# Performance work log

Hardware: AMD Instinct MI355X
Metric: run time of the kernel (lower is better)

## Reference

```python
import jax, jax.numpy as jnp
import numpy as np
from jax import lax

B, L = 2, 2048          # batch, seq_len
V = 256                 # vocab
DM = 256                # d_model
DI = 512                # d_inner = 2*d_model (expand=2)
N = 16                  # d_state
R = 16                  # dt_rank = ceil(d_model/16)
K = 4                   # d_conv
NL = 4                  # n_layer
DO = 10                 # d_output
EPS = 1e-5


def setup_inputs() -> dict:
    key = jax.random.key(0)
    ks = jax.random.split(key, 12)
    f = lambda k, shp, s=0.02: (jax.random.normal(k, shp, jnp.float32) * s)
    A_init = jnp.log(jnp.tile(jnp.arange(1, N + 1, dtype=jnp.float32)[None, None, :], (NL, DI, 1)))
    return {
        "input_ids": jax.random.randint(ks[0], (B, L), 0, V, dtype=jnp.int32),
        "emb": f(ks[1], (V, DM)),
        "norm_w": jnp.ones((NL, DM), jnp.float32),
        "norm_b": jnp.zeros((NL, DM), jnp.float32),
        "in_proj_w": f(ks[2], (NL, 2 * DI, DM)),
        "conv_w": f(ks[3], (NL, DI, K), 0.1),
        "conv_b": jnp.zeros((NL, DI), jnp.float32),
        "x_proj_w": f(ks[4], (NL, R + 2 * N, DI)),
        "dt_proj_w": f(ks[5], (NL, DI, R), 0.1),
        "dt_proj_b": f(ks[6], (NL, DI), 0.1),
        "A_log": A_init,
        "Dp": jnp.ones((NL, DI), jnp.float32),
        "out_proj_w": f(ks[7], (NL, DM, DI)),
        "normf_w": jnp.ones((DM,), jnp.float32),
        "normf_b": jnp.zeros((DM,), jnp.float32),
        "dec_w": f(ks[8], (DO, DM)),
        "dec_b": jnp.zeros((DO,), jnp.float32),
    }


def _layer_norm(x, w, b):
    m = x.mean(-1, keepdims=True)
    v = jnp.mean((x - m) ** 2, axis=-1, keepdims=True)
    return (x - m) * lax.rsqrt(v + EPS) * w + b


def _causal_dwconv(x, w, b):
    # x: [B,L,DI], w: [DI,K] depthwise causal conv
    xt = x.transpose(0, 2, 1)  # [B,DI,L]
    out = lax.conv_general_dilated(xt, w[:, None, :], (1,), [(K - 1, 0)],
                                   feature_group_count=DI)
    return (out + b[None, :, None]).transpose(0, 2, 1)


def _selective_scan(deltaA, deltaBu, C):
    # deltaA, deltaBu: [B,L,DI,N]; C: [B,L,N]
    def step(h, inp):
        dA, dBu, c = inp
        h = dA * h + dBu                       # [B,DI,N]
        y = jnp.einsum('bdn,bn->bd', h, c)
        return h, y
    h0 = jnp.zeros(deltaA.shape[:1] + deltaA.shape[2:], deltaA.dtype)
    _, ys = lax.scan(step, h0, (deltaA.transpose(1, 0, 2, 3),
                                deltaBu.transpose(1, 0, 2, 3),
                                C.transpose(1, 0, 2)))
    return ys.transpose(1, 0, 2)  # [B,L,DI]


def _mixer(x, in_w, cw, cb, xp_w, dt_w, dt_b, A_log, Dp, out_w):
    xz = jnp.einsum('bld,ed->ble', x, in_w)        # [B,L,2*DI]
    xm, z = jnp.split(xz, 2, axis=-1)
    xc = jax.nn.silu(_causal_dwconv(xm, cw, cb))   # [B,L,DI]
    x_dbl = jnp.einsum('bld,ed->ble', xc, xp_w)    # [B,L,R+2N]
    dt, Bm, Cm = jnp.split(x_dbl, [R, R + N], axis=-1)
    delta = jax.nn.softplus(jnp.einsum('blr,dr->bld', dt, dt_w) + dt_b)  # [B,L,DI]
    A = -jnp.exp(A_log)                            # [DI,N]
    deltaA = jnp.exp(delta[..., None] * A)         # [B,L,DI,N]
    deltaBu = delta[..., None] * Bm[:, :, None, :] * xc[..., None]
    y = _selective_scan(deltaA, deltaBu, Cm)       # [B,L,DI]
    y = y + Dp * xc
    y = y * jax.nn.silu(z)
    return jnp.einsum('bld,ed->ble', y, out_w)     # [B,L,DM]


def reference(input_ids, emb, norm_w, norm_b, in_proj_w, conv_w, conv_b,
              x_proj_w, dt_proj_w, dt_proj_b, A_log, Dp, out_proj_w,
              normf_w, normf_b, dec_w, dec_b):
    hidden = emb[input_ids]                        # [B,L,DM]
    residual = None
    for i in range(NL):
        residual = hidden + residual if residual is not None else hidden
        h = _layer_norm(residual, norm_w[i], norm_b[i])
        hidden = _mixer(h, in_proj_w[i], conv_w[i], conv_b[i], x_proj_w[i],
                        dt_proj_w[i], dt_proj_b[i], A_log[i], Dp[i], out_proj_w[i])
    residual = hidden + residual
    hidden = _layer_norm(residual, normf_w, normf_b)
    pooled = hidden.mean(axis=1)                   # [B,DM]
    return pooled @ dec_w.T + dec_b                # [B,DO]
```

## Files before the change

kernel.cpp:

```cpp
#include <hip/hip_runtime.h>
#include <hip/hip_bf16.h>

#define BB 2
#define LL 2048
#define DM 256
#define DI 512
#define NST 16
#define RDT 16
#define KC 4
#define NLAY 4
#define DOUT 10
#define XDIM 48
#define TOK (BB*LL)
#define EPSF 1e-5f
#define CHUNK 16
#define NCH (LL/CHUNK)

typedef __bf16 bf16x8 __attribute__((ext_vector_type(8)));
typedef __bf16 bf16x4 __attribute__((ext_vector_type(4)));
typedef float  f32x4  __attribute__((ext_vector_type(4)));

__device__ __forceinline__ float sigmoid_f(float x) { return 1.0f / (1.0f + __expf(-x)); }

__global__ void cast_w_kernel(const float* __restrict__ a, const float* __restrict__ b,
                              const float* __restrict__ c,
                              __bf16* __restrict__ ab, __bf16* __restrict__ bb,
                              __bf16* __restrict__ cbf,
                              int na, int nb, int nc) {
  int stride = gridDim.x * 256;
  for (int i = blockIdx.x*256 + threadIdx.x; i < na; i += stride) ab[i] = (__bf16)a[i];
  for (int i = blockIdx.x*256 + threadIdx.x; i < nb; i += stride) bb[i] = (__bf16)b[i];
  for (int i = blockIdx.x*256 + threadIdx.x; i < nc; i += stride) cbf[i] = (__bf16)c[i];
}

__global__ void add_ln_kernel(float* __restrict__ residual, const float* __restrict__ hidden,
                              const int* __restrict__ ids, const float* __restrict__ emb,
                              const float* __restrict__ w, const float* __restrict__ bia,
                              float* __restrict__ out, __bf16* __restrict__ out_bf,
                              int first, int write32) {
  int wv = threadIdx.x >> 6, lane = threadIdx.x & 63;
  int t = blockIdx.x*4 + wv;
  float4 rv;
  if (first) {
    rv = *(const float4*)&emb[(size_t)ids[t]*DM + lane*4];
  } else {
    float4 h4 = *(const float4*)&hidden[(size_t)t*DM + lane*4];
    float4 o4 = *(const float4*)&residual[(size_t)t*DM + lane*4];
    rv.x = h4.x + o4.x; rv.y = h4.y + o4.y;
    rv.z = h4.z + o4.z; rv.w = h4.w + o4.w;
  }
  *(float4*)&residual[(size_t)t*DM + lane*4] = rv;
  float s = rv.x + rv.y + rv.z + rv.w;
  #pragma unroll
  for (int o = 32; o; o >>= 1) s += __shfl_xor(s, o);
  float mean = s * (1.0f/DM);
  float d0 = rv.x - mean, d1 = rv.y - mean, d2 = rv.z - mean, d3 = rv.w - mean;
  float q = d0*d0 + d1*d1 + d2*d2 + d3*d3;
  #pragma unroll
  for (int o = 32; o; o >>= 1) q += __shfl_xor(q, o);
  float rsig = rsqrtf(q * (1.0f/DM) + EPSF);
  float4 w4 = *(const float4*)&w[lane*4];
  float4 b4 = *(const float4*)&bia[lane*4];
  float v0 = d0*rsig*w4.x + b4.x;
  float v1 = d1*rsig*w4.y + b4.y;
  float v2 = d2*rsig*w4.z + b4.z;
  float v3 = d3*rsig*w4.w + b4.w;
  if (write32) {
    float4 o4; o4.x = v0; o4.y = v1; o4.z = v2; o4.w = v3;
    *(float4*)&out[(size_t)t*DM + lane*4] = o4;
  }
  bf16x4 bv;
  bv[0] = (__bf16)v0; bv[1] = (__bf16)v1; bv[2] = (__bf16)v2; bv[3] = (__bf16)v3;
  *(bf16x4*)&out_bf[(size_t)t*DM + lane*4] = bv;
}

__global__ __launch_bounds__(256, 2) void gemm_in_bf16(const __bf16* __restrict__ A,
                                                       const __bf16* __restrict__ W,
                                                       __bf16* __restrict__ xm,
                                                       __bf16* __restrict__ zg) {
  __shared__ __bf16 As[4*64*8];
  __shared__ __bf16 Ws[8*64*8];
  const int K = DM;
  int tid = threadIdx.x;
  int lane = tid & 63, wv = tid >> 6;
  int bm = blockIdx.y * 64, be = blockIdx.x * 128;
  int ss = tid >> 6, sq = (tid >> 4) & 3, sm = tid & 15;
  f32x4 acc[8];
  #pragma unroll
  for (int et = 0; et < 8; ++et) acc[et] = (f32x4){0.f, 0.f, 0.f, 0.f};
  for (int k0 = 0; k0 < K; k0 += 32) {
    bf16x8 av = *(const bf16x8*)&A[(size_t)(bm + ss*16 + sm)*K + k0 + sq*8];
    bf16x8 w0 = *(const bf16x8*)&W[(size_t)(be + ss*16 + sm)*K + k0 + sq*8];
    bf16x8 w1 = *(const bf16x8*)&W[(size_t)(be + 64 + ss*16 + sm)*K + k0 + sq*8];
    __syncthreads();
    *(bf16x8*)&As[((ss*4 + sq)*16 + sm)*8] = av;
    *(bf16x8*)&Ws[((ss*4 + sq)*16 + sm)*8] = w0;
    *(bf16x8*)&Ws[(((4 + ss)*4 + sq)*16 + sm)*8] = w1;
    __syncthreads();
    bf16x8 af = *(const bf16x8*)&As[(wv*64 + lane)*8];
    #pragma unroll
    for (int et = 0; et < 8; ++et) {
      bf16x8 bfr = *(const bf16x8*)&Ws[(et*64 + lane)*8];
      acc[et] = __builtin_amdgcn_mfma_f32_16x16x32_bf16(af, bfr, acc[et], 0, 0, 0);
    }
  }
  int row0 = bm + wv*16 + (lane >> 4)*4;
  int colb = lane & 15;
  #pragma unroll
  for (int et = 0; et < 8; ++et) {
    int col = be + et*16 + colb;
    if (col < DI) {
      #pragma unroll
      for (int r = 0; r < 4; ++r)
        xm[(size_t)(row0 + r)*DI + col] = (__bf16)acc[et][r];
    } else {
      #pragma unroll
      for (int r = 0; r < 4; ++r) {
        float zv = acc[et][r];
        zg[(size_t)(row0 + r)*DI + col - DI] = (__bf16)(zv * sigmoid_f(zv));
      }
    }
  }
}

__global__ __launch_bounds__(256, 2) void gemm_out_bf16(const __bf16* __restrict__ A,
                                                        const __bf16* __restrict__ W,
                                                        float* __restrict__ C) {
  __shared__ __bf16 As[4*64*8];
  __shared__ __bf16 Ws[4*64*8];
  const int K = DI, E = DM;
  int tid = threadIdx.x;
  int lane = tid & 63, wv = tid >> 6;
  int bm = blockIdx.y * 64, be = blockIdx.x * 64;
  int ss = tid >> 6, sq = (tid >> 4) & 3, sm = tid & 15;
  f32x4 acc[4];
  #pragma unroll
  for (int et = 0; et < 4; ++et) acc[et] = (f32x4){0.f, 0.f, 0.f, 0.f};
  for (int k0 = 0; k0 < K; k0 += 32) {
    bf16x8 av = *(const bf16x8*)&A[(size_t)(bm + ss*16 + sm)*K + k0 + sq*8];
    bf16x8 wvv = *(const bf16x8*)&W[(size_t)(be + ss*16 + sm)*K + k0 + sq*8];
    __syncthreads();
    *(bf16x8*)&As[((ss*4 + sq)*16 + sm)*8] = av;
    *(bf16x8*)&Ws[((ss*4 + sq)*16 + sm)*8] = wvv;
    __syncthreads();
    bf16x8 af = *(const bf16x8*)&As[(wv*64 + lane)*8];
    #pragma unroll
    for (int et = 0; et < 4; ++et) {
      bf16x8 bfr = *(const bf16x8*)&Ws[(et*64 + lane)*8];
      acc[et] = __builtin_amdgcn_mfma_f32_16x16x32_bf16(af, bfr, acc[et], 0, 0, 0);
    }
  }
  int row0 = bm + wv*16 + (lane >> 4)*4;
  int col0 = be + (lane & 15);
  #pragma unroll
  for (int et = 0; et < 4; ++et)
    #pragma unroll
    for (int r = 0; r < 4; ++r)
      C[(size_t)(row0 + r)*E + col0 + et*16] = acc[et][r];
}

__global__ __launch_bounds__(512) void xproj_scan1(
    const __bf16* __restrict__ xm, const float* __restrict__ cw,
    const float* __restrict__ cb, const __bf16* __restrict__ Wbf,
    const float* __restrict__ dtw, const float* __restrict__ dtb,
    const float* __restrict__ A_log, const float* __restrict__ Dp,
    float* __restrict__ xdbl, float* __restrict__ hloc,
    float* __restrict__ dsum, float* __restrict__ ylocal,
    float* __restrict__ csout) {
  __shared__ float red[8][3][16][16];
  __shared__ __bf16 xc_s[CHUNK][DI];
  __shared__ __align__(16) float DBC[CHUNK][48];
  int tid = threadIdx.x;
  int lane = tid & 63, w = tid >> 6;
  int bc = blockIdx.x;
  int t0 = bc * CHUNK;
  int b = bc >> 7, c = bc & (NCH - 1);
  int r16 = lane & 15;
  int row = t0 + r16;
  int l = row & (LL - 1);
  int kg = (lane >> 4) * 8;

  f32x4 acc[3];
  #pragma unroll
  for (int e = 0; e < 3; ++e) acc[e] = (f32x4){0.f, 0.f, 0.f, 0.f};
  #pragma unroll
  for (int ks = 0; ks < 2; ++ks) {
    int ch = w*64 + ks*32 + kg;
    bf16x8 v0 = *(const bf16x8*)&xm[(size_t)row*DI + ch];
    bf16x8 v1 = (l >= 1) ? *(const bf16x8*)&xm[(size_t)(row-1)*DI + ch] : (bf16x8)(__bf16)0;
    bf16x8 v2 = (l >= 2) ? *(const bf16x8*)&xm[(size_t)(row-2)*DI + ch] : (bf16x8)(__bf16)0;
    bf16x8 v3 = (l >= 3) ? *(const bf16x8*)&xm[(size_t)(row-3)*DI + ch] : (bf16x8)(__bf16)0;
    bf16x8 a8;
    #pragma unroll
    for (int j = 0; j < 8; ++j) {
      float4 cwv = *(const float4*)&cw[(ch + j)*KC];
      float cv = cb[ch + j];
      cv = fmaf(cwv.x, (float)v3[j], cv);
      cv = fmaf(cwv.y, (float)v2[j], cv);
      cv = fmaf(cwv.z, (float)v1[j], cv);
      cv = fmaf(cwv.w, (float)v0[j], cv);
      a8[j] = (__bf16)(cv * sigmoid_f(cv));
    }
    *(bf16x8*)&xc_s[r16][ch ^ ((r16 & 7) << 3)] = a8;
    #pragma unroll
    for (int e = 0; e < 3; ++e) {
      bf16x8 bv = *(const bf16x8*)&Wbf[(size_t)(e*16 + r16)*DI + ch];
      acc[e] = __builtin_amdgcn_mfma_f32_16x16x32_bf16(a8, bv, acc[e], 0, 0, 0);
    }
  }
  #pragma unroll
  for (int e = 0; e < 3; ++e)
    #pragma unroll
    for (int r = 0; r < 4; ++r)
      red[w][e][(lane >> 4)*4 + r][r16] = acc[e][r];
  __syncthreads();
  for (int idx = tid; idx < 768; idx += 512) {
    int e = idx >> 8, rr = (idx >> 4) & 15, cc = idx & 15;
    float s = 0.f;
    #pragma unroll
    for (int w8 = 0; w8 < 8; ++w8) s += red[w8][e][rr][cc];
    DBC[rr][e*16 + cc] = s;
    xdbl[(size_t)(t0 + rr)*XDIM + e*16 + cc] = s;
  }
  __syncthreads();

  int d = tid;
  float4 wq[4];
  #pragma unroll
  for (int i = 0; i < 4; ++i) wq[i] = *(const float4*)&dtw[(size_t)d*RDT + i*4];
  float dtbv = dtb[d];
  float Dpv = Dp[d];
  float A[NST];
  #pragma unroll
  for (int n = 0; n < NST; ++n) A[n] = -__expf(A_log[d*NST + n]);
  float A0 = A[0];
  bool geo = true;
  #pragma unroll
  for (int n = 1; n < NST; ++n) {
    float ideal = A0 * (float)(n+1);
    geo = geo && (fabsf(A[n] - ideal) <= 1e-5f * fabsf(ideal));
  }
  float h[NST];
  #pragma unroll
  for (int n = 0; n < NST; ++n) h[n] = 0.f;
  float ds = 0.f;
  for (int lp = 0; lp < CHUNK; ++lp) {
    int t = t0 + lp;
    float xcv = (float)xc_s[lp][d ^ ((lp & 7) << 3)];
    float acs = dtbv;
    #pragma unroll
    for (int i = 0; i < 4; ++i) {
      float4 a = *(const float4*)&DBC[lp][i*4];
      acs = fmaf(a.x, wq[i].x, acs); acs = fmaf(a.y, wq[i].y, acs);
      acs = fmaf(a.z, wq[i].z, acs); acs = fmaf(a.w, wq[i].w, acs);
    }
    float del = fmaxf(acs, 0.f) + log1pf(__expf(-fabsf(acs)));
    ds += del;
    float dx = del * xcv;
    float yv = 0.f;
    if (geo) {
      float e = __expf(del * A0);
      float dA = e;
      h[0] = fmaf(dA, h[0], dx * DBC[lp][16]);
      yv = fmaf(h[0], DBC[lp][32], yv);
      #pragma unroll
      for (int n = 1; n < NST; ++n) {
        dA *= e;
        h[n] = fmaf(dA, h[n], dx * DBC[lp][16 + n]);
        yv = fmaf(h[n], DBC[lp][32 + n], yv);
      }
    } else {
      #pragma unroll
      for (int n = 0; n < NST; ++n) {
        h[n] = fmaf(__expf(del * A[n]), h[n], dx * DBC[lp][16 + n]);
        yv = fmaf(h[n], DBC[lp][32 + n], yv);
      }
    }
    yv = fmaf(Dpv, xcv, yv);
    ylocal[(size_t)t*DI + d] = yv;
    csout[(size_t)t*DI + d] = ds;
  }
  #pragma unroll
  for (int n = 0; n < NST; ++n)
    hloc[((size_t)(b*NST + n)*NCH + c)*DI + d] = h[n];
  dsum[(size_t)bc*DI + d] = ds;
}

__global__ __launch_bounds__(256) void scan_pass2(
    const float* __restrict__ hloc, const float* __restrict__ dsum,
    const float* __restrict__ A_log, float* __restrict__ hinit) {
  int g = blockIdx.x*256 + threadIdx.x;
  int q = g & 7;
  int chain = g >> 3;
  int d = chain & (DI-1);
  int n = (chain >> 9) & (NST-1);
  int b = chain >> 13;
  float A = -__expf(A_log[d*NST + n]);
  size_t base  = (size_t)(b*NST + n)*NCH*DI + d;
  size_t dbase = (size_t)(b*NCH)*DI + d;
  int c0 = q*16;
  float Pc[16];
  float hc = 0.f, Pp = 1.f;
  #pragma unroll
  for (int i = 0; i < 16; ++i) {
    int cc = c0 + i;
    float P = __expf(A * dsum[dbase + (size_t)cc*DI]);
    Pc[i] = P;
    hc = fmaf(P, hc, hloc[base + (size_t)cc*DI]);
    Pp *= P;
  }
  float Pseg = Pp, Bseg = hc;
  int lane = threadIdx.x & 63;
  int lb = lane & ~7;
  float hin = 0.f;
  #pragma unroll
  for (int j = 0; j < 7; ++j) {
    float Pj = __shfl(Pseg, lb + j);
    float Bj = __shfl(Bseg, lb + j);
    if (j < q) hin = fmaf(Pj, hin, Bj);
  }
  hc = hin;
  #pragma unroll
  for (int i = 0; i < 16; ++i) {
    int cc = c0 + i;
    hinit[base + (size_t)cc*DI] = hc;
    hc = fmaf(Pc[i], hc, hloc[base + (size_t)cc*DI]);
  }
}

__global__ __launch_bounds__(256) void scan_pass3(
    const float* __restrict__ cs, const float* __restrict__ ylocal,
    const __bf16* __restrict__ zg, const float* __restrict__ xdbl,
    const float* __restrict__ A_log, const float* __restrict__ hinit,
    __bf16* __restrict__ y) {
  __shared__ __align__(16) float Cs[CHUNK][16];
  int bc = blockIdx.x >> 1;
  int d  = ((blockIdx.x & 1) << 8) + threadIdx.x;
  int b = bc >> 7, c = bc & (NCH-1);
  int t0 = b*LL + c*CHUNK;
  int tid = threadIdx.x;
  if (tid < CHUNK*4) {
    int row = tid >> 2, q = tid & 3;
    *(float4*)&Cs[row][q*4] = *(const float4*)&xdbl[(size_t)(t0+row)*XDIM + 32 + q*4];
  }
  __syncthreads();
  float A[NST];
  #pragma unroll
  for (int n = 0; n < NST; ++n) A[n] = -__expf(A_log[d*NST + n]);
  float A0 = A[0];
  bool geo = true;
  #pragma unroll
  for (int n = 1; n < NST; ++n) {
    float ideal = A0 * (float)(n+1);
    geo = geo && (fabsf(A[n] - ideal) <= 1e-5f * fabsf(ideal));
  }
  float hin[NST];
  #pragma unroll
  for (int n = 0; n < NST; ++n) hin[n] = hinit[((size_t)(b*NST + n)*NCH + c)*DI + d];
  for (int l = 0; l < CHUNK; ++l) {
    int t = t0 + l;
    float csv = cs[(size_t)t*DI + d];
    float ylv = ylocal[(size_t)t*DI + d];
    float zvg = (float)zg[(size_t)t*DI + d];
    float corr = 0.f;
    if (geo) {
      float g = __expf(csv * A0);
      float dA = g;
      corr = hin[0] * dA * Cs[l][0];
      #pragma unroll
      for (int n = 1; n < NST; ++n) {
        dA *= g;
        corr = fmaf(hin[n] * dA, Cs[l][n], corr);
      }
    } else {
      #pragma unroll
      for (int n = 0; n < NST; ++n)
        corr = fmaf(hin[n] * __expf(A[n] * csv), Cs[l][n], corr);
    }
    y[(size_t)t*DI + d] = (__bf16)((ylv + corr) * zvg);
  }
}

__global__ void pool1_kernel(const float* __restrict__ ln, float* __restrict__ part) {
  int blk = blockIdx.x;
  int b = blk >> 7, c = blk & 127;
  int d = threadIdx.x;
  const float* base = ln + (size_t)b*LL*DM + (size_t)c*16*DM + d;
  float s = 0.f;
  #pragma unroll
  for (int l = 0; l < 16; ++l) s += base[(size_t)l*DM];
  part[(size_t)blk*DM + d] = s;
}

__global__ void pool_decode_kernel(const float* __restrict__ part, const float* __restrict__ dw,
                                   const float* __restrict__ db, float* __restrict__ out) {
  int b = blockIdx.x, d = threadIdx.x;
  __shared__ float pooled[DM];
  float s = 0.f;
  for (int c = 0; c < 128; ++c) s += part[(size_t)(b*128 + c)*DM + d];
  pooled[d] = s * (1.0f/LL);
  __syncthreads();
  if (d < DOUT) {
    float acc = db[d];
    for (int m = 0; m < DM; ++m) acc = fmaf(pooled[m], dw[d*DM + m], acc);
    out[b*DOUT + d] = acc;
  }
}

extern "C" void kernel_launch(void* const* d_in, const int* in_sizes, int n_in,
                              void* d_out, int out_size, void* d_ws, size_t ws_size,
                              hipStream_t stream) {
  const int*   ids     = (const int*)d_in[0];
  const float* emb     = (const float*)d_in[1];
  const float* norm_w  = (const float*)d_in[2];
  const float* norm_b  = (const float*)d_in[3];
  const float* in_w    = (const float*)d_in[4];
  const float* conv_w  = (const float*)d_in[5];
  const float* conv_b  = (const float*)d_in[6];
  const float* xp_w    = (const float*)d_in[7];
  const float* dt_w    = (const float*)d_in[8];
  const float* dt_b    = (const float*)d_in[9];
  const float* A_log   = (const float*)d_in[10];
  const float* Dp      = (const float*)d_in[11];
  const float* out_w   = (const float*)d_in[12];
  const float* normf_w = (const float*)d_in[13];
  const float* normf_b = (const float*)d_in[14];
  const float* dec_w   = (const float*)d_in[15];
  const float* dec_b   = (const float*)d_in[16];
  float* out = (float*)d_out;

  float* ws = (float*)d_ws;
  float* hidden   = ws; ws += TOK*DM;
  float* residual = ws; ws += TOK*DM;
  float* hbuf     = ws; ws += TOK*DM;
  float* xdblbuf  = ws; ws += TOK*XDIM;
  float* hlocbuf  = ws; ws += (size_t)BB*NCH*NST*DI;
  float* hinitbuf = ws; ws += (size_t)BB*NCH*NST*DI;
  float* dsumbuf  = ws; ws += (size_t)BB*NCH*DI;
  float* partbuf  = ws; ws += (size_t)BB*128*DM;
  float* csbuf    = ws; ws += (size_t)TOK*DI;
  float* ylbuf    = ws; ws += (size_t)TOK*DI;
  __bf16* xmbuf   = (__bf16*)ws; ws += TOK*DI/2;
  __bf16* zgbuf   = (__bf16*)ws; ws += TOK*DI/2;
  __bf16* hbuf_bf = (__bf16*)ws; ws += TOK*DM/2;
  __bf16* ybuf_bf = (__bf16*)ws; ws += TOK*DI/2;
  __bf16* inw_bf  = (__bf16*)ws; ws += (size_t)NLAY*2*DI*DM/2;
  __bf16* outw_bf = (__bf16*)ws; ws += (size_t)NLAY*DM*DI/2;
  __bf16* xpw_bf  = (__bf16*)ws; ws += (size_t)NLAY*XDIM*DI/2 + 256;

  const int n_inw = NLAY*2*DI*DM, n_outw = NLAY*DM*DI, n_xpw = NLAY*XDIM*DI;
  cast_w_kernel<<<2048, 256, 0, stream>>>(in_w, out_w, xp_w, inw_bf, outw_bf, xpw_bf,
                                          n_inw, n_outw, n_xpw);

  for (int i = 0; i < NLAY; ++i) {
    add_ln_kernel<<<TOK/4, 256, 0, stream>>>(residual, hidden, ids, emb,
                                             norm_w + i*DM, norm_b + i*DM,
                                             hbuf, hbuf_bf, i == 0, 0);
    gemm_in_bf16<<<dim3((2*DI)/128, TOK/64), 256, 0, stream>>>(
        hbuf_bf, inw_bf + (size_t)i*2*DI*DM, xmbuf, zgbuf);
    xproj_scan1<<<TOK/CHUNK, 512, 0, stream>>>(
        xmbuf, conv_w + i*DI*KC, conv_b + i*DI,
        xpw_bf + (size_t)i*XDIM*DI,
        dt_w + (size_t)i*DI*RDT, dt_b + i*DI, A_log + (size_t)i*DI*NST,
        Dp + i*DI, xdblbuf, hlocbuf, dsumbuf, ylbuf, csbuf);
    scan_pass2<<<(BB*NST*DI*8)/256, 256, 0, stream>>>(
        hlocbuf, dsumbuf, A_log + (size_t)i*DI*NST, hinitbuf);
    scan_pass3<<<BB*NCH*(DI/256), 256, 0, stream>>>(
        csbuf, ylbuf, zgbuf, xdblbuf, A_log + (size_t)i*DI*NST,
        hinitbuf, ybuf_bf);
    gemm_out_bf16<<<dim3(DM/64, TOK/64), 256, 0, stream>>>(
        ybuf_bf, outw_bf + (size_t)i*DM*DI, hidden);
  }

  add_ln_kernel<<<TOK/4, 256, 0, stream>>>(residual, hidden, ids, emb,
                                           normf_w, normf_b, hbuf, hbuf_bf, 0, 1);
  pool1_kernel<<<BB*128, DM, 0, stream>>>(hbuf, partbuf);
  pool_decode_kernel<<<BB, DM, 0, stream>>>(partbuf, dec_w, dec_b, out);
}
```

Before: 370.4 us.

## Drop LDS staging in GEMMs, fuse final pooling into layernorm, trim xdbl writes

The in/out projection GEMMs now load A and W fragments directly from global memory into MFMA operands, with no shared-memory staging and no block barriers. The final layernorm reduces each block's four tokens in shared memory and writes partial sums, which removes the fp32 LN output buffer and the separate pool1 kernel. pool_decode now sums TOK/4 partials per batch instead of 128. xproj_scan1 writes only the C slice of xdbl, presumably the only part read later. Direct global loads give up LDS reuse across waves and rely on L1/L2 hits, and the decode reduction becomes more serial.

```diff
diff --git a/kernel.cpp b/kernel.cpp
--- a/kernel.cpp
+++ b/kernel.cpp
@@ -36,8 +36,9 @@
 __global__ void add_ln_kernel(float* __restrict__ residual, const float* __restrict__ hidden,
                               const int* __restrict__ ids, const float* __restrict__ emb,
                               const float* __restrict__ w, const float* __restrict__ bia,
-                              float* __restrict__ out, __bf16* __restrict__ out_bf,
-                              int first, int write32) {
+                              __bf16* __restrict__ out_bf, float* __restrict__ part,
+                              int first, int mode) {
+  __shared__ float ps[4][DM];
   int wv = threadIdx.x >> 6, lane = threadIdx.x & 63;
   int t = blockIdx.x*4 + wv;
   float4 rv;
@@ -65,43 +66,40 @@
   float v1 = d1*rsig*w4.y + b4.y;
   float v2 = d2*rsig*w4.z + b4.z;
   float v3 = d3*rsig*w4.w + b4.w;
-  if (write32) {
-    float4 o4; o4.x = v0; o4.y = v1; o4.z = v2; o4.w = v3;
-    *(float4*)&out[(size_t)t*DM + lane*4] = o4;
-  }
-  bf16x4 bv;
-  bv[0] = (__bf16)v0; bv[1] = (__bf16)v1; bv[2] = (__bf16)v2; bv[3] = (__bf16)v3;
-  *(bf16x4*)&out_bf[(size_t)t*DM + lane*4] = bv;
+  if (mode) {
+    ps[wv][lane*4 + 0] = v0; ps[wv][lane*4 + 1] = v1;
+    ps[wv][lane*4 + 2] = v2; ps[wv][lane*4 + 3] = v3;
+    __syncthreads();
+    int tid = threadIdx.x;
+    float sm = ps[0][tid] + ps[1][tid] + ps[2][tid] + ps[3][tid];
+    part[(size_t)blockIdx.x*DM + tid] = sm;
+  } else {
+    bf16x4 bv;
+    bv[0] = (__bf16)v0; bv[1] = (__bf16)v1; bv[2] = (__bf16)v2; bv[3] = (__bf16)v3;
+    *(bf16x4*)&out_bf[(size_t)t*DM + lane*4] = bv;
+  }
 }
 
 __global__ __launch_bounds__(256, 2) void gemm_in_bf16(const __bf16* __restrict__ A,
                                                        const __bf16* __restrict__ W,
                                                        __bf16* __restrict__ xm,
                                                        __bf16* __restrict__ zg) {
-  __shared__ __bf16 As[4*64*8];
-  __shared__ __bf16 Ws[8*64*8];
   const int K = DM;
   int tid = threadIdx.x;
   int lane = tid & 63, wv = tid >> 6;
   int bm = blockIdx.y * 64, be = blockIdx.x * 128;
-  int ss = tid >> 6, sq = (tid >> 4) & 3, sm = tid & 15;
+  int arow = bm + wv*16 + (lane & 15);
+  int wrow = lane & 15;
+  int kg = (lane >> 4) * 8;
   f32x4 acc[8];
   #pragma unroll
   for (int et = 0; et < 8; ++et) acc[et] = (f32x4){0.f, 0.f, 0.f, 0.f};
   for (int k0 = 0; k0 < K; k0 += 32) {
-    bf16x8 av = *(const bf16x8*)&A[(size_t)(bm + ss*16 + sm)*K + k0 + sq*8];
-    bf16x8 w0 = *(const bf16x8*)&W[(size_t)(be + ss*16 + sm)*K + k0 + sq*8];
-    bf16x8 w1 = *(const bf16x8*)&W[(size_t)(be + 64 + ss*16 + sm)*K + k0 + sq*8];
-    __syncthreads();
-    *(bf16x8*)&As[((ss*4 + sq)*16 + sm)*8] = av;
-    *(bf16x8*)&Ws[((ss*4 + sq)*16 + sm)*8] = w0;
-    *(bf16x8*)&Ws[(((4 + ss)*4 + sq)*16 + sm)*8] = w1;
-    __syncthreads();
-    bf16x8 af = *(const bf16x8*)&As[(wv*64 + lane)*8];
+    bf16x8 av = *(const bf16x8*)&A[(size_t)arow*K + k0 + kg];
     #pragma unroll
     for (int et = 0; et < 8; ++et) {
-      bf16x8 bfr = *(const bf16x8*)&Ws[(et*64 + lane)*8];
-      acc[et] = __builtin_amdgcn_mfma_f32_16x16x32_bf16(af, bfr, acc[et], 0, 0, 0);
+      bf16x8 bv = *(const bf16x8*)&W[(size_t)(be + et*16 + wrow)*K + k0 + kg];
+      acc[et] = __builtin_amdgcn_mfma_f32_16x16x32_bf16(av, bv, acc[et], 0, 0, 0);
     }
   }
   int row0 = bm + wv*16 + (lane >> 4)*4;
@@ -126,28 +124,22 @@
 __global__ __launch_bounds__(256, 2) void gemm_out_bf16(const __bf16* __restrict__ A,
                                                         const __bf16* __restrict__ W,
                                                         float* __restrict__ C) {
-  __shared__ __bf16 As[4*64*8];
-  __shared__ __bf16 Ws[4*64*8];
   const int K = DI, E = DM;
   int tid = threadIdx.x;
   int lane = tid & 63, wv = tid >> 6;
   int bm = blockIdx.y * 64, be = blockIdx.x * 64;
-  int ss = tid >> 6, sq = (tid >> 4) & 3, sm = tid & 15;
+  int arow = bm + wv*16 + (lane & 15);
+  int wrow = lane & 15;
+  int kg = (lane >> 4) * 8;
   f32x4 acc[4];
   #pragma unroll
   for (int et = 0; et < 4; ++et) acc[et] = (f32x4){0.f, 0.f, 0.f, 0.f};
   for (int k0 = 0; k0 < K; k0 += 32) {
-    bf16x8 av = *(const bf16x8*)&A[(size_t)(bm + ss*16 + sm)*K + k0 + sq*8];
-    bf16x8 wvv = *(const bf16x8*)&W[(size_t)(be + ss*16 + sm)*K + k0 + sq*8];
-    __syncthreads();
-    *(bf16x8*)&As[((ss*4 + sq)*16 + sm)*8] = av;
-    *(bf16x8*)&Ws[((ss*4 + sq)*16 + sm)*8] = wvv;
-    __syncthreads();
-    bf16x8 af = *(const bf16x8*)&As[(wv*64 + lane)*8];
+    bf16x8 av = *(const bf16x8*)&A[(size_t)arow*K + k0 + kg];
     #pragma unroll
     for (int et = 0; et < 4; ++et) {
-      bf16x8 bfr = *(const bf16x8*)&Ws[(et*64 + lane)*8];
-      acc[et] = __builtin_amdgcn_mfma_f32_16x16x32_bf16(af, bfr, acc[et], 0, 0, 0);
+      bf16x8 bv = *(const bf16x8*)&W[(size_t)(be + et*16 + wrow)*K + k0 + kg];
+      acc[et] = __builtin_amdgcn_mfma_f32_16x16x32_bf16(av, bv, acc[et], 0, 0, 0);
     }
   }
   int row0 = bm + wv*16 + (lane >> 4)*4;
@@ -220,7 +212,7 @@
     #pragma unroll
     for (int w8 = 0; w8 < 8; ++w8) s += red[w8][e][rr][cc];
     DBC[rr][e*16 + cc] = s;
-    xdbl[(size_t)(t0 + rr)*XDIM + e*16 + cc] = s;
+    if (e == 2) xdbl[(size_t)(t0 + rr)*XDIM + 32 + cc] = s;
   }
   __syncthreads();
 
@@ -381,23 +373,12 @@
   }
 }
 
-__global__ void pool1_kernel(const float* __restrict__ ln, float* __restrict__ part) {
-  int blk = blockIdx.x;
-  int b = blk >> 7, c = blk & 127;
-  int d = threadIdx.x;
-  const float* base = ln + (size_t)b*LL*DM + (size_t)c*16*DM + d;
-  float s = 0.f;
-  #pragma unroll
-  for (int l = 0; l < 16; ++l) s += base[(size_t)l*DM];
-  part[(size_t)blk*DM + d] = s;
-}
-
 __global__ void pool_decode_kernel(const float* __restrict__ part, const float* __restrict__ dw,
                                    const float* __restrict__ db, float* __restrict__ out) {
   int b = blockIdx.x, d = threadIdx.x;
   __shared__ float pooled[DM];
   float s = 0.f;
-  for (int c = 0; c < 128; ++c) s += part[(size_t)(b*128 + c)*DM + d];
+  for (int c = 0; c < LL/4; ++c) s += part[(size_t)(b*(LL/4) + c)*DM + d];
   pooled[d] = s * (1.0f/LL);
   __syncthreads();
   if (d < DOUT) {
@@ -432,12 +413,11 @@
   float* ws = (float*)d_ws;
   float* hidden   = ws; ws += TOK*DM;
   float* residual = ws; ws += TOK*DM;
-  float* hbuf     = ws; ws += TOK*DM;
   float* xdblbuf  = ws; ws += TOK*XDIM;
   float* hlocbuf  = ws; ws += (size_t)BB*NCH*NST*DI;
   float* hinitbuf = ws; ws += (size_t)BB*NCH*NST*DI;
   float* dsumbuf  = ws; ws += (size_t)BB*NCH*DI;
-  float* partbuf  = ws; ws += (size_t)BB*128*DM;
+  float* partbuf  = ws; ws += (size_t)(TOK/4)*DM;
   float* csbuf    = ws; ws += (size_t)TOK*DI;
   float* ylbuf    = ws; ws += (size_t)TOK*DI;
   __bf16* xmbuf   = (__bf16*)ws; ws += TOK*DI/2;
@@ -455,7 +435,7 @@
   for (int i = 0; i < NLAY; ++i) {
     add_ln_kernel<<<TOK/4, 256, 0, stream>>>(residual, hidden, ids, emb,
                                              norm_w + i*DM, norm_b + i*DM,
-                                             hbuf, hbuf_bf, i == 0, 0);
+                                             hbuf_bf, partbuf, i == 0, 0);
     gemm_in_bf16<<<dim3((2*DI)/128, TOK/64), 256, 0, stream>>>(
         hbuf_bf, inw_bf + (size_t)i*2*DI*DM, xmbuf, zgbuf);
     xproj_scan1<<<TOK/CHUNK, 512, 0, stream>>>(
@@ -473,7 +453,6 @@
   }
 
   add_ln_kernel<<<TOK/4, 256, 0, stream>>>(residual, hidden, ids, emb,
-                                           normf_w, normf_b, hbuf, hbuf_bf, 0, 1);
-  pool1_kernel<<<BB*128, DM, 0, stream>>>(hbuf, partbuf);
+                                           normf_w, normf_b, hbuf_bf, partbuf, 0, 1);
   pool_decode_kernel<<<BB, DM, 0, stream>>>(partbuf, dec_w, dec_b, out);
 }
```

Result: slower. 421.4 us (+13.8%).
